# Optimization experiments

Hardware: AMD Instinct MI355X
Metric: run time of the kernel (lower is better)

## Reference

```python
import jax, jax.numpy as jnp
import numpy as np

DIM = 768
HEADS = 12
WS = 8       # window_size
EPS = 1e-5   # torch LayerNorm eps


def _ln(x, g, b):
    m = jnp.mean(x, axis=-1, keepdims=True)
    v = jnp.var(x, axis=-1, keepdims=True)
    return (x - m) / jnp.sqrt(v + EPS) * g + b


def _attention(xw, qkv_w, proj_w, proj_b):
    # xw: (Bw, N, C) with N = WS*WS
    Bw, N, C = xw.shape
    D = C // HEADS
    scale = D ** -0.5
    # torch does x.reshape(3, B, N, C//3): a flat row-major split, identical in jax
    x3 = xw.reshape(3, Bw, N, C // 3)
    def tile(t):  # cat((t,t,t)) then reshape(B,N,C), exactly as torch
        return jnp.concatenate([t, t, t], axis=0).reshape(Bw, N, C)
    red, green, blue = tile(x3[0]), tile(x3[1]), tile(x3[2])
    # qkv Linear has no bias (qkv_bias=False); only k,v of Red and q of Green/Blue
    # are used, and q_green + q_blue == (green+blue) @ Wq^T
    Wq, Wk, Wv = qkv_w[:C], qkv_w[C:2 * C], qkv_w[2 * C:]
    def heads(t):  # (Bw,N,C) -> (Bw,H,N,D)
        return t.reshape(Bw, N, HEADS, D).transpose(0, 2, 1, 3)
    q = heads((green + blue) @ Wq.T)
    k = heads(red @ Wk.T)
    v = heads(red @ Wv.T)
    attn = jax.nn.softmax(jnp.einsum('bhnd,bhmd->bhnm', q, k) * scale, axis=-1)
    out = jnp.einsum('bhnm,bhmd->bhnd', attn, v).transpose(0, 2, 1, 3).reshape(Bw, N, C)
    return out @ proj_w.T + proj_b


def setup_inputs() -> dict:
    key = jax.random.key(0)
    ks = jax.random.split(key, 6)
    B, H, W, C = 4, 128, 128, DIM
    def p(k, shape):
        return jax.random.normal(k, shape, jnp.float32) * 0.02
    return {
        'x': jax.random.normal(ks[0], (B, H * W, C), jnp.float32),
        'norm1_g': jnp.ones((C,), jnp.float32),
        'norm1_b': jnp.zeros((C,), jnp.float32),
        'norm2_g': jnp.ones((C,), jnp.float32),
        'norm2_b': jnp.zeros((C,), jnp.float32),
        'qkv_w': p(ks[1], (3 * C, C)),
        'proj_w': p(ks[2], (C, C)),
        'proj_b': jnp.zeros((C,), jnp.float32),
        'fc1_w': p(ks[3], (1, C)),   # Mlp hidden_features hardcoded to 1 in source
        'fc1_b': jnp.zeros((1,), jnp.float32),
        'fc2_w': p(ks[4], (C, 1)),
        'fc2_b': jnp.zeros((C,), jnp.float32),
        'h': 128,
        'w': 128,
    }


def reference(x, norm1_g, norm1_b, norm2_g, norm2_b, qkv_w, proj_w, proj_b,
              fc1_w, fc1_b, fc2_w, fc2_b, h, w):
    B, L, C = x.shape
    xn = _ln(x, norm1_g, norm1_b).reshape(B, h, w, C)
    # window_partition: (B,H,W,C) -> (nW*B, WS*WS, C)
    xw = xn.reshape(B, h // WS, WS, w // WS, WS, C)
    xw = xw.transpose(0, 1, 3, 2, 4, 5).reshape(-1, WS * WS, C)
    a = _attention(xw, qkv_w, proj_w, proj_b)
    a = _ln(a, norm2_g, norm2_b)
    # NOTE: source has NO residual connections; output is mlp(norm2(attn(...)))
    hdn = jax.nn.gelu(a @ fc1_w.T + fc1_b, approximate=False)  # torch GELU = exact erf
    m = hdn @ fc2_w.T + fc2_b
    return m.reshape(B, h * w, C)
```

## Files before the change

kernel.cpp:

```cpp
#include <hip/hip_runtime.h>
#include <hip/hip_bf16.h>
#include <stdint.h>
#include <stddef.h>

typedef __bf16 bf16;
typedef __bf16 bf16x4 __attribute__((ext_vector_type(4)));
typedef __bf16 bf16x8 __attribute__((ext_vector_type(8)));
typedef float  f32x4  __attribute__((ext_vector_type(4)));

__device__ __forceinline__ void async16(const void* src, void* dst) {
    __builtin_amdgcn_global_load_lds(
        (__attribute__((address_space(1))) void*)(void*)(src),
        (__attribute__((address_space(3))) void*)(dst),
        16, 0, 0);
}

__global__ __launch_bounds__(256)
void f2b(const float* __restrict__ src, bf16* __restrict__ dst, int n)
{
    const int i = (blockIdx.x * 256 + threadIdx.x) * 4;
    if (i < n) {
        f32x4 c = *(const f32x4*)(src + i);
        bf16x4 o;
        #pragma unroll
        for (int q = 0; q < 4; ++q) o[q] = (bf16)c[q];
        *(bf16x4*)(dst + i) = o;
    }
}

__global__ __launch_bounds__(256)
void ln1_win(const float* __restrict__ x, const float* __restrict__ g,
             const float* __restrict__ b, bf16* __restrict__ Y)
{
    const int row  = blockIdx.x * 4 + (threadIdx.x >> 6);
    const int lane = threadIdx.x & 63;
    const float* xr = x + (size_t)row * 768;
    float v[12];
    float sum = 0.f, ssq = 0.f;
    #pragma unroll
    for (int j = 0; j < 3; ++j) {
        f32x4 c = *(const f32x4*)(xr + j * 256 + lane * 4);
        #pragma unroll
        for (int q = 0; q < 4; ++q) {
            float f = c[q];
            v[j * 4 + q] = f; sum += f; ssq += f * f;
        }
    }
    #pragma unroll
    for (int d = 1; d < 64; d <<= 1) {
        sum += __shfl_xor(sum, d, 64);
        ssq += __shfl_xor(ssq, d, 64);
    }
    const float mean = sum * (1.f / 768.f);
    const float rstd = rsqrtf(ssq * (1.f / 768.f) - mean * mean + 1e-5f);
    const int bb = row >> 14;
    const int l  = row & 16383;
    const int hy = l >> 7, wx = l & 127;
    const int m  = ((bb * 256 + (hy >> 3) * 16 + (wx >> 3)) << 6)
                 + ((hy & 7) << 3) + (wx & 7);
    bf16* yr = Y + (size_t)m * 768;
    #pragma unroll
    for (int j = 0; j < 3; ++j) {
        const int c0 = j * 256 + lane * 4;
        f32x4 gg = *(const f32x4*)(g + c0);
        f32x4 bv = *(const f32x4*)(b + c0);
        bf16x4 ov;
        #pragma unroll
        for (int q = 0; q < 4; ++q)
            ov[q] = (bf16)((v[j * 4 + q] - mean) * rstd * gg[q] + bv[q]);
        *(bf16x4*)(yr + c0) = ov;
    }
}

template<int AMODE, bool BIAS>
__global__ __launch_bounds__(256, 2)
void gemm_bt(const bf16* __restrict__ A, const bf16* __restrict__ Yg,
             const bf16* __restrict__ Bm, const float* __restrict__ bias,
             bf16* __restrict__ Cm, int K, int ldc, int Smod, int nb_n)
{
    __shared__ bf16 At[128 * 64];
    __shared__ bf16 Bt[256 * 64];

    const int per    = gridDim.x >> 3;
    const int mchunk = per / nb_n;
    const int xcd    = blockIdx.x & 7;
    const int slot_b = blockIdx.x >> 3;
    const int mbase  = (xcd * mchunk + slot_b / nb_n) * 128;
    const int nbase  = (slot_b % nb_n) * 256;

    const int tid  = threadIdx.x;
    const int lane = tid & 63;
    const int w    = tid >> 6;
    const int quad = lane >> 4;
    const int l16  = lane & 15;
    const int wm   = (w >> 1) * 64;
    const int wn   = (w & 1) * 128;

    const f32x4 zero = {0.f, 0.f, 0.f, 0.f};
    f32x4 acc[4][8];
    #pragma unroll
    for (int i = 0; i < 4; ++i)
        #pragma unroll
        for (int j = 0; j < 8; ++j) acc[i][j] = zero;

    const bool qpath = (AMODE == 1) && (nbase < 768);

    for (int kb = 0; kb < K; kb += 64) {
        {
            const int rb   = 64 * w;
            const int rsub = lane >> 3;
            const int slot = lane & 7;
            #pragma unroll
            for (int t = 0; t < 8; ++t) {
                const int row = rb + 8 * t + rsub;
                const int kc  = slot ^ (row & 7);
                async16(Bm + (size_t)(nbase + row) * K + kb + kc * 8,
                        Bt + (rb + 8 * t) * 64);
            }
        }
        if (AMODE == 0) {
            const int rb   = 32 * w;
            const int rsub = lane >> 3;
            const int slot = lane & 7;
            #pragma unroll
            for (int t = 0; t < 4; ++t) {
                const int row = rb + 8 * t + rsub;
                const int kc  = slot ^ (row & 7);
                async16(A + (size_t)(mbase + row) * K + kb + kc * 8,
                        At + (rb + 8 * t) * 64);
            }
        } else if (qpath) {
            #pragma unroll
            for (int t = 0; t < 4; ++t) {
                const int c    = tid + 256 * t;
                const int row  = c >> 3;
                const int slot = c & 7;
                const int kc   = slot ^ (row & 7);
                int f = (mbase + row) * 768 + kb + kc * 8;
                if (f >= 2 * Smod) f -= 2 * Smod;
                else if (f >= Smod) f -= Smod;
                bf16x8 u  = *(const bf16x8*)(Yg + Smod + f);
                bf16x8 vv = *(const bf16x8*)(Yg + 2 * Smod + f);
                bf16x8 r;
                #pragma unroll
                for (int q = 0; q < 8; ++q)
                    r[q] = (bf16)((float)u[q] + (float)vv[q]);
                *(bf16x8*)(At + row * 64 + slot * 8) = r;
            }
        } else {
            const int rb   = 32 * w;
            const int rsub = lane >> 3;
            const int slot = lane & 7;
            #pragma unroll
            for (int t = 0; t < 4; ++t) {
                const int row = rb + 8 * t + rsub;
                const int kc  = slot ^ (row & 7);
                int f = (mbase + row) * 768 + kb + kc * 8;
                if (f >= 2 * Smod) f -= 2 * Smod;
                else if (f >= Smod) f -= Smod;
                async16(Yg + f, At + (rb + 8 * t) * 64);
            }
        }
        __syncthreads();

        #pragma unroll
        for (int ks = 0; ks < 2; ++ks) {
            bf16x8 af[4], bfr[8];
            #pragma unroll
            for (int i = 0; i < 4; ++i) {
                const int row  = wm + 16 * i + l16;
                const int slot = (ks * 4 + quad) ^ (row & 7);
                af[i] = *(const bf16x8*)(At + row * 64 + slot * 8);
            }
            #pragma unroll
            for (int j = 0; j < 8; ++j) {
                const int row  = wn + 16 * j + l16;
                const int slot = (ks * 4 + quad) ^ (row & 7);
                bfr[j] = *(const bf16x8*)(Bt + row * 64 + slot * 8);
            }
            #pragma unroll
            for (int i = 0; i < 4; ++i)
                #pragma unroll
                for (int j = 0; j < 8; ++j)
                    acc[i][j] = __builtin_amdgcn_mfma_f32_16x16x32_bf16(
                        af[i], bfr[j], acc[i][j], 0, 0, 0);
        }
        __syncthreads();
    }

    #pragma unroll
    for (int i = 0; i < 4; ++i) {
        const int row0 = mbase + wm + 16 * i + quad * 4;
        #pragma unroll
        for (int j = 0; j < 8; ++j) {
            const int col = nbase + wn + 16 * j + l16;
            float bv = 0.f;
            if (BIAS) bv = bias[col];
            #pragma unroll
            for (int r = 0; r < 4; ++r)
                Cm[(size_t)(row0 + r) * ldc + col] = (bf16)(acc[i][j][r] + bv);
        }
    }
}

__global__ __launch_bounds__(64)
void attn_win(const bf16* __restrict__ QKV, bf16* __restrict__ AOut)
{
    const int blk  = blockIdx.x;
    const int bw   = blk / 12;
    const int h    = blk % 12;
    const int lane = threadIdx.x;
    const int quad = lane >> 4;
    const int l16  = lane & 15;

    __shared__ bf16 Kt[64 * 64];
    __shared__ bf16 Vt[64 * 64];

    const size_t rowbase = (size_t)bw * 64;

    {
        const int rsub = lane >> 3;
        const int slot = lane & 7;
        #pragma unroll
        for (int t = 0; t < 8; ++t) {
            const int row = 8 * t + rsub;
            const int kcK = slot ^ (row & 7);
            async16(QKV + (rowbase + row) * 2304 + 768 + h * 64 + kcK * 8,
                    Kt + (8 * t) * 64);
            async16(QKV + (rowbase + row) * 2304 + 1536 + h * 64 + slot * 8,
                    Vt + (8 * t) * 64);
        }
    }

    bf16x8 qf[4][2];
    #pragma unroll
    for (int i = 0; i < 4; ++i)
        #pragma unroll
        for (int ks = 0; ks < 2; ++ks)
            qf[i][ks] = *(const bf16x8*)(QKV + (rowbase + 16 * i + l16) * 2304
                                         + h * 64 + ks * 32 + quad * 8);
    __syncthreads();

    const f32x4 zero = {0.f, 0.f, 0.f, 0.f};
    f32x4 s[4][4];
    #pragma unroll
    for (int i = 0; i < 4; ++i)
        #pragma unroll
        for (int j = 0; j < 4; ++j) s[i][j] = zero;

    #pragma unroll
    for (int ks = 0; ks < 2; ++ks) {
        bf16x8 kf[4];
        #pragma unroll
        for (int j = 0; j < 4; ++j) {
            const int row  = 16 * j + l16;
            const int slot = (ks * 4 + quad) ^ (row & 7);
            kf[j] = *(const bf16x8*)(Kt + row * 64 + slot * 8);
        }
        #pragma unroll
        for (int i = 0; i < 4; ++i)
            #pragma unroll
            for (int j = 0; j < 4; ++j)
                s[i][j] = __builtin_amdgcn_mfma_f32_16x16x32_bf16(
                    qf[i][ks], kf[j], s[i][j], 0, 0, 0);
    }

    float rrec[4][4];
    #pragma unroll
    for (int i = 0; i < 4; ++i) {
        #pragma unroll
        for (int r = 0; r < 4; ++r) {
            float mx = s[i][0][r];
            #pragma unroll
            for (int j = 1; j < 4; ++j) mx = fmaxf(mx, s[i][j][r]);
            #pragma unroll
            for (int d = 1; d < 16; d <<= 1) mx = fmaxf(mx, __shfl_xor(mx, d, 64));
            float sum = 0.f;
            #pragma unroll
            for (int j = 0; j < 4; ++j) {
                float p = __expf((s[i][j][r] - mx) * 0.125f);
                s[i][j][r] = p;
                sum += p;
            }
            #pragma unroll
            for (int d = 1; d < 16; d <<= 1) sum += __shfl_xor(sum, d, 64);
            rrec[i][r] = 1.f / sum;
        }
    }

    #pragma unroll
    for (int i = 0; i < 4; ++i)
        #pragma unroll
        for (int j = 0; j < 4; ++j)
            #pragma unroll
            for (int r = 0; r < 4; ++r) {
                const int row  = 16 * i + quad * 4 + r;
                const int col  = 16 * j + l16;
                const int slot = (col >> 3) ^ (row & 7);
                Kt[row * 64 + slot * 8 + (col & 7)] = (bf16)s[i][j][r];
            }
    __syncthreads();

    f32x4 o[4][4];
    #pragma unroll
    for (int i = 0; i < 4; ++i)
        #pragma unroll
        for (int j = 0; j < 4; ++j) o[i][j] = zero;

    #pragma unroll
    for (int ks = 0; ks < 2; ++ks) {
        bf16x8 pf[4], vf[4];
        #pragma unroll
        for (int i = 0; i < 4; ++i) {
            const int row  = 16 * i + l16;
            const int slot = (ks * 4 + quad) ^ (row & 7);
            pf[i] = *(const bf16x8*)(Kt + row * 64 + slot * 8);
        }
        #pragma unroll
        for (int j = 0; j < 4; ++j) {
            bf16x8 t;
            #pragma unroll
            for (int q = 0; q < 8; ++q)
                t[q] = Vt[(ks * 32 + quad * 8 + q) * 64 + 16 * j + l16];
            vf[j] = t;
        }
        #pragma unroll
        for (int i = 0; i < 4; ++i)
            #pragma unroll
            for (int j = 0; j < 4; ++j)
                o[i][j] = __builtin_amdgcn_mfma_f32_16x16x32_bf16(
                    pf[i], vf[j], o[i][j], 0, 0, 0);
    }

    #pragma unroll
    for (int i = 0; i < 4; ++i)
        #pragma unroll
        for (int j = 0; j < 4; ++j)
            #pragma unroll
            for (int r = 0; r < 4; ++r) {
                const size_t grow = rowbase + 16 * i + quad * 4 + r;
                const int col = h * 64 + 16 * j + l16;
                AOut[grow * 768 + col] = (bf16)(o[i][j][r] * rrec[i][r]);
            }
}

__global__ __launch_bounds__(256)
void final_fused(const bf16* __restrict__ P, const float* __restrict__ g2,
                 const float* __restrict__ b2, const float* __restrict__ fc1w,
                 const float* __restrict__ fc1b, const float* __restrict__ fc2w,
                 const float* __restrict__ fc2b, float* __restrict__ out)
{
    const int row  = blockIdx.x * 4 + (threadIdx.x >> 6);
    const int lane = threadIdx.x & 63;
    const bf16* pr = P + (size_t)row * 768;
    float v[12];
    float sum = 0.f, ssq = 0.f;
    #pragma unroll
    for (int j = 0; j < 3; ++j) {
        bf16x4 c = *(const bf16x4*)(pr + j * 256 + lane * 4);
        #pragma unroll
        for (int q = 0; q < 4; ++q) {
            float f = (float)c[q];
            v[j * 4 + q] = f; sum += f; ssq += f * f;
        }
    }
    #pragma unroll
    for (int d = 1; d < 64; d <<= 1) {
        sum += __shfl_xor(sum, d, 64);
        ssq += __shfl_xor(ssq, d, 64);
    }
    const float mean = sum * (1.f / 768.f);
    const float rstd = rsqrtf(ssq * (1.f / 768.f) - mean * mean + 1e-5f);
    float part = 0.f;
    #pragma unroll
    for (int j = 0; j < 3; ++j) {
        const int c0 = j * 256 + lane * 4;
        f32x4 gg = *(const f32x4*)(g2 + c0);
        f32x4 bb = *(const f32x4*)(b2 + c0);
        f32x4 f1 = *(const f32x4*)(fc1w + c0);
        #pragma unroll
        for (int q = 0; q < 4; ++q) {
            float ln = (v[j * 4 + q] - mean) * rstd * gg[q] + bb[q];
            part += ln * f1[q];
        }
    }
    #pragma unroll
    for (int d = 1; d < 64; d <<= 1) part += __shfl_xor(part, d, 64);
    const float sv = part + fc1b[0];
    const float ge = 0.5f * sv * (1.f + erff(sv * 0.70710678118654752f));
    float* orow = out + (size_t)row * 768;
    #pragma unroll
    for (int j = 0; j < 3; ++j) {
        const int c0 = j * 256 + lane * 4;
        f32x4 f2  = *(const f32x4*)(fc2w + c0);
        f32x4 b2v = *(const f32x4*)(fc2b + c0);
        f32x4 ov;
        #pragma unroll
        for (int q = 0; q < 4; ++q)
            ov[q] = ge * f2[q] + b2v[q];
        *(f32x4*)(orow + c0) = ov;
    }
}

extern "C" void kernel_launch(void* const* d_in, const int* in_sizes, int n_in,
                              void* d_out, int out_size, void* d_ws, size_t ws_size,
                              hipStream_t stream)
{
    const float* x     = (const float*)d_in[0];
    const float* n1g   = (const float*)d_in[1];
    const float* n1b   = (const float*)d_in[2];
    const float* n2g   = (const float*)d_in[3];
    const float* n2b   = (const float*)d_in[4];
    const float* qkvw  = (const float*)d_in[5];
    const float* projw = (const float*)d_in[6];
    const float* projb = (const float*)d_in[7];
    const float* fc1w  = (const float*)d_in[8];
    const float* fc1b  = (const float*)d_in[9];
    const float* fc2w  = (const float*)d_in[10];
    const float* fc2b  = (const float*)d_in[11];
    float* out = (float*)d_out;

    const int total = in_sizes[0];
    const int rows  = total / 768;
    const int Smod  = total / 3;
    const int Bw    = rows / 64;
    const int C     = 768;

    bf16* qkv     = (bf16*)d_ws;
    bf16* Ybuf    = qkv + (size_t)rows * 2304;
    bf16* qkvw_b  = Ybuf + (size_t)rows * 768;
    bf16* projw_b = qkvw_b + (size_t)3 * C * C;
    bf16* Pbuf    = qkv;

    const int nqkvw  = 3 * C * C;
    const int nprojw = C * C;
    f2b<<<(nqkvw / 4 + 255) / 256, 256, 0, stream>>>(qkvw, qkvw_b, nqkvw);
    f2b<<<(nprojw / 4 + 255) / 256, 256, 0, stream>>>(projw, projw_b, nprojw);

    ln1_win<<<rows / 4, 256, 0, stream>>>(x, n1g, n1b, Ybuf);

    const int nbm = rows / 128;
    gemm_bt<1, false><<<nbm * 9, 256, 0, stream>>>(
        nullptr, Ybuf, qkvw_b, nullptr, qkv, 768, 2304, Smod, 9);

    attn_win<<<Bw * 12, 64, 0, stream>>>(qkv, Ybuf);

    gemm_bt<0, true><<<nbm * 3, 256, 0, stream>>>(
        Ybuf, nullptr, projw_b, projb, Pbuf, 768, 768, 0, 3);

    final_fused<<<rows / 4, 256, 0, stream>>>(Pbuf, n2g, n2b, fc1w, fc1b,
                                              fc2w, fc2b, out);
}
```

Measured before the change: 856.2 us.

## Triple-buffer GEMM with async LDS loads, 512 threads, and a precomputed green+blue sum

The GEMM now uses 8 waves with 64x64 per-wave tiles and a three-stage LDS ring. Loads for the next tiles are issued while the current tile computes, with explicit vmcnt waits and raw barriers instead of the single-stage load/sync/compute loop. The green+blue sum for the Q path moves out of the GEMM into a separate gsum kernel that writes into the output buffer as scratch, so every A-tile load can use async global-to-LDS copies. It also adds nontemporal stores for the QKV output and s_setprio around the MFMA blocks. In exchange it costs an extra kernel pass over a third of the activations and much more LDS (about 144KB per block), which may limit occupancy.

```diff
diff --git a/kernel.cpp b/kernel.cpp
--- a/kernel.cpp
+++ b/kernel.cpp
@@ -14,6 +14,8 @@
         (__attribute__((address_space(3))) void*)(dst),
         16, 0, 0);
 }
+
+#define MEMFENCE asm volatile("" ::: "memory")
 
 __global__ __launch_bounds__(256)
 void f2b(const float* __restrict__ src, bf16* __restrict__ dst, int n)
@@ -72,14 +74,31 @@
     }
 }
 
-template<int AMODE, bool BIAS>
-__global__ __launch_bounds__(256, 2)
+__global__ __launch_bounds__(256)
+void gsum(const bf16* __restrict__ Y, bf16* __restrict__ G, int Smod)
+{
+    const int i = (blockIdx.x * 256 + threadIdx.x) * 8;
+    if (i < Smod) {
+        bf16x8 a = *(const bf16x8*)(Y + Smod + i);
+        bf16x8 c = *(const bf16x8*)(Y + 2 * Smod + i);
+        bf16x8 r;
+        #pragma unroll
+        for (int q = 0; q < 8; ++q) r[q] = (bf16)((float)a[q] + (float)c[q]);
+        *(bf16x8*)(G + i) = r;
+    }
+}
+
+template<int AMODE, bool BIAS, bool NT>
+__global__ __launch_bounds__(512, 2)
 void gemm_bt(const bf16* __restrict__ A, const bf16* __restrict__ Yg,
-             const bf16* __restrict__ Bm, const float* __restrict__ bias,
-             bf16* __restrict__ Cm, int K, int ldc, int Smod, int nb_n)
-{
-    __shared__ bf16 At[128 * 64];
-    __shared__ bf16 Bt[256 * 64];
+             const bf16* __restrict__ Gb, const bf16* __restrict__ Bm,
+             const float* __restrict__ bias, bf16* __restrict__ Cm,
+             int K, int ldc, int Smod, int nb_n)
+{
+    constexpr int ABUF = 128 * 64;
+    constexpr int BBUF = 256 * 64;
+    constexpr int BUF  = ABUF + BBUF;
+    __shared__ bf16 lds[3 * BUF];
 
     const int per    = gridDim.x >> 3;
     const int mchunk = per / nb_n;
@@ -93,112 +112,125 @@
     const int w    = tid >> 6;
     const int quad = lane >> 4;
     const int l16  = lane & 15;
-    const int wm   = (w >> 1) * 64;
-    const int wn   = (w & 1) * 128;
+    const int wm   = (w >> 2) * 64;
+    const int wn   = (w & 3) * 64;
+    const int rsub = lane >> 3;
+    const int slot = lane & 7;
+
+    const bf16* Asrc = (AMODE == 1) ? ((nbase < 768) ? Gb : Yg) : A;
+    const int nt = K >> 6;
+
+    auto stageA = [&](int t, int kt, bf16* Ab) {
+        const int row = 16 * w + 8 * t + rsub;
+        const int kc  = slot ^ (row & 7);
+        const bf16* s;
+        if (AMODE == 1) {
+            int f = (mbase + row) * 768 + kt * 64 + kc * 8;
+            if (f >= 2 * Smod) f -= 2 * Smod;
+            else if (f >= Smod) f -= Smod;
+            s = Asrc + f;
+        } else {
+            s = Asrc + (size_t)(mbase + row) * K + kt * 64 + kc * 8;
+        }
+        async16(s, Ab + (16 * w + 8 * t) * 64);
+    };
+    auto stageB = [&](int t, int kt, bf16* Bb) {
+        const int row = 32 * w + 8 * t + rsub;
+        const int kc  = slot ^ (row & 7);
+        async16(Bm + (size_t)(nbase + row) * K + kt * 64 + kc * 8,
+                Bb + (32 * w + 8 * t) * 64);
+    };
 
     const f32x4 zero = {0.f, 0.f, 0.f, 0.f};
-    f32x4 acc[4][8];
-    #pragma unroll
-    for (int i = 0; i < 4; ++i)
-        #pragma unroll
-        for (int j = 0; j < 8; ++j) acc[i][j] = zero;
-
-    const bool qpath = (AMODE == 1) && (nbase < 768);
-
-    for (int kb = 0; kb < K; kb += 64) {
-        {
-            const int rb   = 64 * w;
-            const int rsub = lane >> 3;
-            const int slot = lane & 7;
-            #pragma unroll
-            for (int t = 0; t < 8; ++t) {
-                const int row = rb + 8 * t + rsub;
-                const int kc  = slot ^ (row & 7);
-                async16(Bm + (size_t)(nbase + row) * K + kb + kc * 8,
-                        Bt + (rb + 8 * t) * 64);
-            }
-        }
-        if (AMODE == 0) {
-            const int rb   = 32 * w;
-            const int rsub = lane >> 3;
-            const int slot = lane & 7;
-            #pragma unroll
-            for (int t = 0; t < 4; ++t) {
-                const int row = rb + 8 * t + rsub;
-                const int kc  = slot ^ (row & 7);
-                async16(A + (size_t)(mbase + row) * K + kb + kc * 8,
-                        At + (rb + 8 * t) * 64);
-            }
-        } else if (qpath) {
-            #pragma unroll
-            for (int t = 0; t < 4; ++t) {
-                const int c    = tid + 256 * t;
-                const int row  = c >> 3;
-                const int slot = c & 7;
-                const int kc   = slot ^ (row & 7);
-                int f = (mbase + row) * 768 + kb + kc * 8;
-                if (f >= 2 * Smod) f -= 2 * Smod;
-                else if (f >= Smod) f -= Smod;
-                bf16x8 u  = *(const bf16x8*)(Yg + Smod + f);
-                bf16x8 vv = *(const bf16x8*)(Yg + 2 * Smod + f);
-                bf16x8 r;
-                #pragma unroll
-                for (int q = 0; q < 8; ++q)
-                    r[q] = (bf16)((float)u[q] + (float)vv[q]);
-                *(bf16x8*)(At + row * 64 + slot * 8) = r;
-            }
+    f32x4 acc[4][4];
+    #pragma unroll
+    for (int i = 0; i < 4; ++i)
+        #pragma unroll
+        for (int j = 0; j < 4; ++j) acc[i][j] = zero;
+
+    auto compute = [&](int ks, const bf16* Ab, const bf16* Bb) {
+        bf16x8 af[4], bfr[4];
+        #pragma unroll
+        for (int i = 0; i < 4; ++i) {
+            const int row = wm + 16 * i + l16;
+            const int sl  = (ks * 4 + quad) ^ (row & 7);
+            af[i] = *(const bf16x8*)(Ab + row * 64 + sl * 8);
+        }
+        #pragma unroll
+        for (int j = 0; j < 4; ++j) {
+            const int row = wn + 16 * j + l16;
+            const int sl  = (ks * 4 + quad) ^ (row & 7);
+            bfr[j] = *(const bf16x8*)(Bb + row * 64 + sl * 8);
+        }
+        __builtin_amdgcn_s_setprio(1);
+        #pragma unroll
+        for (int i = 0; i < 4; ++i)
+            #pragma unroll
+            for (int j = 0; j < 4; ++j)
+                acc[i][j] = __builtin_amdgcn_mfma_f32_16x16x32_bf16(
+                    af[i], bfr[j], acc[i][j], 0, 0, 0);
+        __builtin_amdgcn_s_setprio(0);
+    };
+
+    {
+        bf16* Ab = lds;        bf16* Bb = lds + ABUF;
+        stageA(0, 0, Ab); stageA(1, 0, Ab);
+        stageB(0, 0, Bb); stageB(1, 0, Bb); stageB(2, 0, Bb); stageB(3, 0, Bb);
+        if (nt > 1) {
+            bf16* A1 = lds + BUF; bf16* B1 = lds + BUF + ABUF;
+            stageA(0, 1, A1); stageA(1, 1, A1);
+            stageB(0, 1, B1); stageB(1, 1, B1); stageB(2, 1, B1); stageB(3, 1, B1);
+            asm volatile("s_waitcnt vmcnt(6)" ::: "memory");
         } else {
-            const int rb   = 32 * w;
-            const int rsub = lane >> 3;
-            const int slot = lane & 7;
-            #pragma unroll
-            for (int t = 0; t < 4; ++t) {
-                const int row = rb + 8 * t + rsub;
-                const int kc  = slot ^ (row & 7);
-                int f = (mbase + row) * 768 + kb + kc * 8;
-                if (f >= 2 * Smod) f -= 2 * Smod;
-                else if (f >= Smod) f -= Smod;
-                async16(Yg + f, At + (rb + 8 * t) * 64);
-            }
-        }
-        __syncthreads();
-
-        #pragma unroll
-        for (int ks = 0; ks < 2; ++ks) {
-            bf16x8 af[4], bfr[8];
-            #pragma unroll
-            for (int i = 0; i < 4; ++i) {
-                const int row  = wm + 16 * i + l16;
-                const int slot = (ks * 4 + quad) ^ (row & 7);
-                af[i] = *(const bf16x8*)(At + row * 64 + slot * 8);
-            }
-            #pragma unroll
-            for (int j = 0; j < 8; ++j) {
-                const int row  = wn + 16 * j + l16;
-                const int slot = (ks * 4 + quad) ^ (row & 7);
-                bfr[j] = *(const bf16x8*)(Bt + row * 64 + slot * 8);
-            }
-            #pragma unroll
-            for (int i = 0; i < 4; ++i)
-                #pragma unroll
-                for (int j = 0; j < 8; ++j)
-                    acc[i][j] = __builtin_amdgcn_mfma_f32_16x16x32_bf16(
-                        af[i], bfr[j], acc[i][j], 0, 0, 0);
-        }
-        __syncthreads();
+            asm volatile("s_waitcnt vmcnt(0)" ::: "memory");
+        }
+    }
+    __builtin_amdgcn_s_barrier();
+    MEMFENCE;
+
+    int cur = 0;
+    for (int t = 0; t < nt; ++t) {
+        bf16* Ab = lds + cur * BUF;
+        bf16* Bb = Ab + ABUF;
+        const int nx = (cur + 2 >= 3) ? cur - 1 : cur + 2;
+        bf16* An = lds + nx * BUF;
+        bf16* Bn = An + ABUF;
+        const bool pf = (t + 2 < nt);
+
+        if (pf) { stageA(0, t + 2, An); stageB(0, t + 2, Bn); stageB(1, t + 2, Bn); }
+        compute(0, Ab, Bb);
+        __builtin_amdgcn_s_barrier();
+        MEMFENCE;
+
+        if (pf) { stageA(1, t + 2, An); stageB(2, t + 2, Bn); stageB(3, t + 2, Bn); }
+        compute(1, Ab, Bb);
+        if (t < nt - 2) { asm volatile("s_waitcnt vmcnt(6)" ::: "memory"); }
+        else            { asm volatile("s_waitcnt vmcnt(0)" ::: "memory"); }
+        __builtin_amdgcn_s_barrier();
+        MEMFENCE;
+
+        cur = (cur + 1 == 3) ? 0 : cur + 1;
     }
 
     #pragma unroll
     for (int i = 0; i < 4; ++i) {
         const int row0 = mbase + wm + 16 * i + quad * 4;
         #pragma unroll
-        for (int j = 0; j < 8; ++j) {
+        for (int j = 0; j < 4; ++j) {
             const int col = nbase + wn + 16 * j + l16;
             float bv = 0.f;
             if (BIAS) bv = bias[col];
             #pragma unroll
-            for (int r = 0; r < 4; ++r)
-                Cm[(size_t)(row0 + r) * ldc + col] = (bf16)(acc[i][j][r] + bv);
+            for (int r = 0; r < 4; ++r) {
+                bf16 val = (bf16)(acc[i][j][r] + bv);
+                bf16* p = Cm + (size_t)(row0 + r) * ldc + col;
+                if (NT) {
+                    unsigned short u = __builtin_bit_cast(unsigned short, val);
+                    __builtin_nontemporal_store(u, (unsigned short*)p);
+                } else {
+                    *p = val;
+                }
+            }
         }
     }
 }
@@ -431,6 +463,7 @@
     bf16* qkvw_b  = Ybuf + (size_t)rows * 768;
     bf16* projw_b = qkvw_b + (size_t)3 * C * C;
     bf16* Pbuf    = qkv;
+    bf16* Gb      = (bf16*)d_out;
 
     const int nqkvw  = 3 * C * C;
     const int nprojw = C * C;
@@ -439,14 +472,16 @@
 
     ln1_win<<<rows / 4, 256, 0, stream>>>(x, n1g, n1b, Ybuf);
 
+    gsum<<<(Smod / 8 + 255) / 256, 256, 0, stream>>>(Ybuf, Gb, Smod);
+
     const int nbm = rows / 128;
-    gemm_bt<1, false><<<nbm * 9, 256, 0, stream>>>(
-        nullptr, Ybuf, qkvw_b, nullptr, qkv, 768, 2304, Smod, 9);
+    gemm_bt<1, false, true><<<nbm * 9, 512, 0, stream>>>(
+        nullptr, Ybuf, Gb, qkvw_b, nullptr, qkv, 768, 2304, Smod, 9);
 
     attn_win<<<Bw * 12, 64, 0, stream>>>(qkv, Ybuf);
 
-    gemm_bt<0, true><<<nbm * 3, 256, 0, stream>>>(
-        Ybuf, nullptr, projw_b, projb, Pbuf, 768, 768, 0, 3);
+    gemm_bt<0, true, false><<<nbm * 3, 512, 0, stream>>>(
+        Ybuf, nullptr, nullptr, projw_b, projb, Pbuf, 768, 768, 0, 3);
 
     final_fused<<<rows / 4, 256, 0, stream>>>(Pbuf, n2g, n2b, fc1w, fc1b,
                                               fc2w, fc2b, out);
```

After: 909.0 us. 6.2% more time.
